# Kernel optimization log

Measured on AMD Instinct MI355X. Metric: run time of the kernel, lower is better.

The kernel has to match this reference:

```python
import jax, jax.numpy as jnp
import numpy as np
import math

B, S, D = 16, 577, 768          # batch, seq (24*24 grid + 1 cls), in_dim=att_dim
H, HD = 12, 64                  # heads, head_dim
GRID = 24                       # height = width; S = GRID*GRID + rpe_skip
RATIO = 1.9
ALPHA, BETA, GAMMA = 1.0 * RATIO, 2.0 * RATIO, 8.0 * RATIO
BETA_INT = int(BETA)            # 3
NUM_BUCKETS = (2 * BETA_INT + 1) ** 2 + 1  # 49 product buckets + 1 extra for skip (cls) = 50


def _piecewise_index(d):
    # iRPE piecewise bucket index (numpy, static). d: integer offsets.
    d = d.astype(np.float64)
    ad = np.abs(d)
    log_part = ALPHA + np.log(np.maximum(ad, 1e-9) / ALPHA) / math.log(GAMMA / ALPHA) * (BETA - ALPHA)
    y_out = np.sign(d) * np.clip(np.round(log_part), None, BETA)
    idx = np.where(ad <= ALPHA, np.round(d), y_out)
    return np.trunc(idx).astype(np.int64)  # torch .to(int) truncates toward zero


def make_rp_bucket():
    # 2D 'product' method bucket ids with skip=1 (cls token -> extra bucket)
    ii, jj = np.meshgrid(np.arange(GRID), np.arange(GRID), indexing='ij')
    pos = np.stack([ii.ravel(), jj.ravel()], axis=-1)          # (L,2)
    diff = pos[:, None, :] - pos[None, :, :]                    # (L,L,2)
    Sb = 2 * BETA_INT + 1
    r = _piecewise_index(diff[..., 0]) + BETA_INT               # [0, 2*beta_int]
    c = _piecewise_index(diff[..., 1]) + BETA_INT
    pid = r * Sb + c                                            # [0, 48]
    L = GRID * GRID
    bucket = np.full((L + 1, L + 1), NUM_BUCKETS - 1, dtype=np.int32)
    bucket[1:, 1:] = pid
    return jnp.asarray(bucket)


def setup_inputs() -> dict:
    key = jax.random.key(0)
    k1, k2, k3 = jax.random.split(key, 3)
    x = jax.random.normal(k1, (B, S, D), dtype=jnp.float32)
    w_qkv = jax.random.normal(k2, (3 * D, D), dtype=jnp.float32) * 0.02   # torch Linear weight (out,in)
    rpe_table = jax.random.normal(k3, (HD, NUM_BUCKETS), dtype=jnp.float32) * 0.02  # shared-head contextual table
    rp_bucket = make_rp_bucket()                                # (S,S) int32
    return {"x": x, "w_qkv": w_qkv, "rpe_table": rpe_table, "rp_bucket": rp_bucket}


def reference(x, w_qkv, rpe_table, rp_bucket):
    qkv = x @ w_qkv.T                                           # (B,S,3D)
    q, k, v = jnp.split(qkv, 3, axis=-1)
    # Faithful to torch source: plain reshape (B,S,D)->(B,H,S,HD) (no transpose-split)
    scale = 1.0 / jnp.sqrt(jnp.asarray(HD, x.dtype))
    q = q.reshape(B, H, S, HD) * scale
    k = k.reshape(B, H, S, HD)
    v = v.reshape(B, H, S, HD)
    qk = jnp.einsum('bhid,bhjd->bhij', q, k)                    # (B,H,S,S)
    # contextual rpe_k: bias[b,h,i,j] = (q[b,h,i] . rpe_table[:, rp_bucket[i,j]])
    ctx = jnp.einsum('bhid,dc->bhic', q, rpe_table)             # (B,H,S,NUM_BUCKETS)
    idx = jnp.broadcast_to(rp_bucket[None, None].astype(jnp.int32), (B, H, S, S))
    bias = jnp.take_along_axis(ctx, idx, axis=-1)               # (B,H,S,S)
    att = jax.nn.softmax(qk + bias, axis=-1)
    out = jnp.einsum('bhij,bhjd->bhid', att, v)                 # (B,H,S,HD)
    y = out.transpose(0, 2, 1, 3).reshape(B, S, D)              # out_proj is Identity (out_dim==att_dim)
    return y
```

## Files before the change

kernel.cpp:

```cpp
#include <hip/hip_runtime.h>

constexpr int BN_  = 16;
constexpr int SN_  = 577;
constexpr int SP_  = 640;
constexpr int DN_  = 768;
constexpr int HN_  = 12;
constexpr int HD_  = 64;
constexpr int NB_  = 50;
constexpr int MR_  = BN_ * SN_;
constexpr int MRP_ = 73 * 128;
constexpr int NQ_  = 3 * DN_;
constexpr int BHS_ = BN_ * HN_ * SN_;
constexpr int SHD_ = SN_ * HD_;

typedef __attribute__((ext_vector_type(8))) short short8;
typedef __attribute__((ext_vector_type(4))) float f32x4;

__device__ __forceinline__ short f2bf(float f) {
  union { float f; unsigned u; } v; v.f = f;
  unsigned r = (v.u + 0x7fffu + ((v.u >> 16) & 1u)) >> 16;
  return (short)r;
}

__device__ __forceinline__ float ex2(float x) {
  float r; asm("v_exp_f32 %0, %1" : "=v"(r) : "v"(x)); return r;
}

__launch_bounds__(256)
__global__ void cvt_k(const float* __restrict__ src, short* __restrict__ dst,
                      int n_src, int n_dst) {
  const int i = (blockIdx.x * 256 + threadIdx.x) * 8;
  if (i >= n_dst) return;
  union { short8 v; short u[8]; } pk;
  if (i < n_src) {
    const float4 a = *(const float4*)(src + i);
    const float4 b = *(const float4*)(src + i + 4);
    pk.u[0] = f2bf(a.x); pk.u[1] = f2bf(a.y); pk.u[2] = f2bf(a.z); pk.u[3] = f2bf(a.w);
    pk.u[4] = f2bf(b.x); pk.u[5] = f2bf(b.y); pk.u[6] = f2bf(b.z); pk.u[7] = f2bf(b.w);
  } else {
#pragma unroll
    for (int j = 0; j < 8; ++j) pk.u[j] = 0;
  }
  *(short8*)(dst + i) = pk.v;
}

__launch_bounds__(256)
__global__ void rpb8_k(const int* __restrict__ rpb, unsigned char* __restrict__ rpbu8) {
  const int tid = blockIdx.x * 256 + threadIdx.x;
  if (tid >= SN_ * 160) return;
  const int i = tid / 160, c4 = tid - i * 160;
  const int j = c4 * 4;
  uchar4 o;
  o.x = (j     < SN_) ? (unsigned char)rpb[i * SN_ + j    ] : 0;
  o.y = (j + 1 < SN_) ? (unsigned char)rpb[i * SN_ + j + 1] : 0;
  o.z = (j + 2 < SN_) ? (unsigned char)rpb[i * SN_ + j + 2] : 0;
  o.w = (j + 3 < SN_) ? (unsigned char)rpb[i * SN_ + j + 3] : 0;
  *(uchar4*)(rpbu8 + (size_t)i * 640 + j) = o;
}

__launch_bounds__(256)
__global__ void qkv_mfma_k(const short* __restrict__ xb, const short* __restrict__ wb,
                           short* __restrict__ Qbf, short* __restrict__ Ksw,
                           short* __restrict__ Vbf) {
  __shared__ short At[128 * 64];
  __shared__ short Bt[128 * 64];
  const int t = threadIdx.x;
  const int w = t >> 6, lane = t & 63, g = lane >> 4, ln = lane & 15;
  const int wm = w >> 1, wn = w & 1;
  const int m0 = blockIdx.y * 128, n0 = blockIdx.x * 128;

  const int sr = t >> 1, su = (t & 1) * 4;
  const short* ga = xb + (size_t)(m0 + sr) * DN_ + su * 8;
  const short* gb = wb + (size_t)(n0 + sr) * DN_ + su * 8;
  short* la = At + sr * 64;
  short* lb = Bt + sr * 64;
  const int swr = sr & 7;

  f32x4 acc[4][4];
#pragma unroll
  for (int mt = 0; mt < 4; ++mt)
#pragma unroll
    for (int nt = 0; nt < 4; ++nt) acc[mt][nt] = (f32x4){0.f, 0.f, 0.f, 0.f};

  short8 ra[4], rb[4];
#pragma unroll
  for (int u = 0; u < 4; ++u) {
    ra[u] = *(const short8*)(ga + u * 8);
    rb[u] = *(const short8*)(gb + u * 8);
  }

  for (int k0 = 0; k0 < DN_; k0 += 64) {
    __syncthreads();
#pragma unroll
    for (int u = 0; u < 4; ++u) {
      *(short8*)(la + (((su + u) ^ swr) * 8)) = ra[u];
      *(short8*)(lb + (((su + u) ^ swr) * 8)) = rb[u];
    }
    __syncthreads();
    if (k0 + 64 < DN_) {
#pragma unroll
      for (int u = 0; u < 4; ++u) {
        ra[u] = *(const short8*)(ga + k0 + 64 + u * 8);
        rb[u] = *(const short8*)(gb + k0 + 64 + u * 8);
      }
    }
#pragma unroll
    for (int kc = 0; kc < 2; ++kc) {
      short8 af[4], bf[4];
#pragma unroll
      for (int mt = 0; mt < 4; ++mt) {
        const int row = wm * 64 + mt * 16 + ln;
        const int u = (kc * 4 + g) ^ (row & 7);
        af[mt] = *(const short8*)&At[row * 64 + u * 8];
      }
#pragma unroll
      for (int nt = 0; nt < 4; ++nt) {
        const int row = wn * 64 + nt * 16 + ln;
        const int u = (kc * 4 + g) ^ (row & 7);
        bf[nt] = *(const short8*)&Bt[row * 64 + u * 8];
      }
#pragma unroll
      for (int mt = 0; mt < 4; ++mt)
#pragma unroll
        for (int nt = 0; nt < 4; ++nt)
          acc[mt][nt] = __builtin_amdgcn_mfma_f32_16x16x32_bf16(af[mt], bf[nt], acc[mt][nt], 0, 0, 0);
    }
  }

  const int nw0  = n0 + wn * 64;
  const int secg = nw0 / DN_;
  const int cbw  = nw0 - secg * DN_;
  const float QSC = 0.18033688011112042f;
#pragma unroll
  for (int mt = 0; mt < 4; ++mt) {
#pragma unroll
    for (int r = 0; r < 4; ++r) {
      const int gm = m0 + wm * 64 + mt * 16 + 4 * g + r;
      if (gm >= MR_) continue;
      const int bb = gm / SN_;
      const int ss = gm - bb * SN_;
      const int pb = ss * DN_ + cbw;
#pragma unroll
      for (int nt = 0; nt < 4; ++nt) {
        const int p   = pb + nt * 16 + ln;
        const int hh  = p / SHD_;
        const int rem = p - hh * SHD_;
        const int ii  = rem >> 6;
        const int dd  = rem & 63;
        const size_t ro = (size_t)(bb * HN_ + hh);
        const float v = acc[mt][nt][r];
        if (secg == 0) {
          Qbf[(ro * SN_ + ii) * 64 + dd] = f2bf(v * QSC);
        } else if (secg == 1) {
          Ksw[(ro * SP_ + ii) * 64 + (dd ^ ((ii & 7) << 3))] = f2bf(v);
        } else {
          Vbf[(ro * SP_ + ii) * 64 + dd] = f2bf(v);
        }
      }
    }
  }
}

__launch_bounds__(256)
__global__ void vtr_k(const short* __restrict__ Vbf, short* __restrict__ Vtsw) {
  __shared__ short T[64][72];
  const int t = threadIdx.x;
  const int jt = blockIdx.x, bh = blockIdx.y;
  const int j0 = jt * 64;
  {
    const int r = t >> 2, c0 = (t & 3) * 16;
    const short* src = Vbf + ((size_t)bh * SP_ + j0 + r) * 64 + c0;
    *(short8*)&T[r][c0]     = *(const short8*)(src);
    *(short8*)&T[r][c0 + 8] = *(const short8*)(src + 8);
  }
  __syncthreads();
  const int d = t >> 2;
  short* dst = Vtsw + ((size_t)bh * 64 + d) * SP_;
  const int sw = (d & 7) << 3;
#pragma unroll
  for (int e = 0; e < 4; ++e) {
    const int jl = (t & 3) * 16 + e * 4;
    const int jg = j0 + jl;
    short4 v;
    v.x = (jg + 0 < SN_) ? T[jl + 0][d] : (short)0;
    v.y = (jg + 1 < SN_) ? T[jl + 1][d] : (short)0;
    v.z = (jg + 2 < SN_) ? T[jl + 2][d] : (short)0;
    v.w = (jg + 3 < SN_) ? T[jl + 3][d] : (short)0;
    *(short4*)&dst[jg ^ sw] = v;
  }
}

__launch_bounds__(256)
__global__ void attn_k(const short* __restrict__ Qbf, const short* __restrict__ Ksw,
                       const short* __restrict__ Vtsw, const float* __restrict__ rpe,
                       const unsigned char* __restrict__ rpbu8, float* __restrict__ y) {
  __shared__ short Kt[64 * 64];
  __shared__ short Vt[64 * 64];
  __shared__ float ctxs[4][16][53];
  __shared__ char urp[8192];
  short (*Rp)[64] = (short (*)[64])urp;
  unsigned char* rpbt = (unsigned char*)urp;

  const int t = threadIdx.x;
  const int w = t >> 6, lane = t & 63, g = lane >> 4, ln = lane & 15;
  const int qt = blockIdx.x, bh = blockIdx.y;
  const int b = bh / HN_, h = bh - b * HN_;
  const int i0 = qt * 64;
  const size_t rb = (size_t)bh * SN_;
  const short* Kbh = Ksw + (size_t)bh * SP_ * 64;
  const short* Vbh = Vtsw + (size_t)bh * 64 * SP_;

  const int sr_ = t >> 2, scu_ = (t & 3) * 16;
  const int irow_s = (i0 + sr_ <= SN_ - 1) ? (i0 + sr_) : (SN_ - 1);

  short8 kr0, kr1, vr0, vr1; int4 rp_;
  {
    const short* ks = Kbh + (size_t)sr_ * 64 + scu_;
    kr0 = *(const short8*)(ks); kr1 = *(const short8*)(ks + 8);
    const short* vs = Vbh + (size_t)sr_ * SP_ + scu_;
    vr0 = *(const short8*)(vs); vr1 = *(const short8*)(vs + 8);
    rp_ = *(const int4*)(rpbu8 + (size_t)irow_s * 640 + scu_);
  }

  for (int e = t; e < 64 * 64; e += 256) {
    const int c = e >> 6, d = e & 63;
    Rp[c][d] = (c < NB_) ? f2bf(rpe[d * NB_ + c]) : (short)0;
  }

  short8 qf[2];
  {
    int row = i0 + 16 * w + ln; if (row > SN_ - 1) row = SN_ - 1;
    const short* qp = Qbf + (rb + row) * 64;
    qf[0] = *(const short8*)(qp + 8 * g);
    qf[1] = *(const short8*)(qp + 32 + 8 * g);
  }

  __syncthreads();

  {
    f32x4 accC[4];
#pragma unroll
    for (int ct = 0; ct < 4; ++ct) accC[ct] = (f32x4){0.f, 0.f, 0.f, 0.f};
#pragma unroll
    for (int kc = 0; kc < 2; ++kc) {
#pragma unroll
      for (int ct = 0; ct < 4; ++ct) {
        const short8 rf = *(const short8*)&Rp[ct * 16 + ln][kc * 32 + 8 * g];
        accC[ct] = __builtin_amdgcn_mfma_f32_16x16x32_bf16(qf[kc], rf, accC[ct], 0, 0, 0);
      }
    }
#pragma unroll
    for (int ct = 0; ct < 4; ++ct) {
      const int c = ct * 16 + ln;
      if (c < 53) {
#pragma unroll
        for (int r = 0; r < 4; ++r) ctxs[w][4 * g + r][c] = accC[ct][r];
      }
    }
  }

  float m = -3e38f, l = 0.f;
  f32x4 accO[4];
#pragma unroll
  for (int dt = 0; dt < 4; ++dt) accO[dt] = (f32x4){0.f, 0.f, 0.f, 0.f};

  const int swv = (ln & 7) << 3;
  const float* cbase = &ctxs[w][ln][0];
  const int rpoff = (16 * w + ln) * 80;

  for (int jt = 0; jt < 10; ++jt) {
    const int j0 = jt * 64;
    __syncthreads();
    *(short8*)&Kt[sr_ * 64 + scu_]     = kr0;
    *(short8*)&Kt[sr_ * 64 + scu_ + 8] = kr1;
    *(short8*)&Vt[sr_ * 64 + scu_]     = vr0;
    *(short8*)&Vt[sr_ * 64 + scu_ + 8] = vr1;
    *(int4*)&rpbt[sr_ * 80 + scu_]     = rp_;
    __syncthreads();

    if (jt < 9) {
      const int jn = j0 + 64;
      const short* ks = Kbh + (size_t)(jn + sr_) * 64 + scu_;
      kr0 = *(const short8*)(ks); kr1 = *(const short8*)(ks + 8);
      const short* vs = Vbh + (size_t)sr_ * SP_ + jn + scu_;
      vr0 = *(const short8*)(vs); vr1 = *(const short8*)(vs + 8);
      rp_ = *(const int4*)(rpbu8 + (size_t)irow_s * 640 + jn + scu_);
    }

    f32x4 accS[4];
#pragma unroll
    for (int nt = 0; nt < 4; ++nt) accS[nt] = (f32x4){0.f, 0.f, 0.f, 0.f};
#pragma unroll
    for (int kc = 0; kc < 2; ++kc) {
      const int cb = (kc * 32 + 8 * g) ^ swv;
#pragma unroll
      for (int nt = 0; nt < 4; ++nt) {
        const short8 kf = *(const short8*)&Kt[(nt * 16 + ln) * 64 + cb];
        accS[nt] = __builtin_amdgcn_mfma_f32_16x16x32_bf16(kf, qf[kc], accS[nt], 0, 0, 0);
      }
    }

    float pv[4][4];
#pragma unroll
    for (int nt = 0; nt < 4; ++nt) {
      const uchar4 bk = *(const uchar4*)&rpbt[rpoff + nt * 16 + 4 * g];
      pv[nt][0] = accS[nt][0] + cbase[bk.x];
      pv[nt][1] = accS[nt][1] + cbase[bk.y];
      pv[nt][2] = accS[nt][2] + cbase[bk.z];
      pv[nt][3] = accS[nt][3] + cbase[bk.w];
    }
    if (jt == 9) {
#pragma unroll
      for (int nt = 0; nt < 4; ++nt) {
        const int jb = j0 + nt * 16 + 4 * g;
#pragma unroll
        for (int r = 0; r < 4; ++r)
          if (jb + r >= SN_) pv[nt][r] = -3e38f;
      }
    }

    float mx = fmaxf(fmaxf(pv[0][0], pv[0][1]), fmaxf(pv[0][2], pv[0][3]));
#pragma unroll
    for (int nt = 1; nt < 4; ++nt)
      mx = fmaxf(mx, fmaxf(fmaxf(pv[nt][0], pv[nt][1]), fmaxf(pv[nt][2], pv[nt][3])));
    mx = fmaxf(mx, __shfl_xor(mx, 16));
    mx = fmaxf(mx, __shfl_xor(mx, 32));

    if (__any(mx > m + 8.f)) {
      const float mnew = fmaxf(m, mx);
      const float sc = ex2(m - mnew);
      float scr[4];
#pragma unroll
      for (int r = 0; r < 4; ++r) scr[r] = __shfl(sc, 4 * g + r);
#pragma unroll
      for (int dt = 0; dt < 4; ++dt)
#pragma unroll
        for (int r = 0; r < 4; ++r) accO[dt][r] *= scr[r];
      l *= sc;
      m = mnew;
    }

    float sum = 0.f;
#pragma unroll
    for (int nt = 0; nt < 4; ++nt)
#pragma unroll
      for (int r = 0; r < 4; ++r) {
        const float p = ex2(pv[nt][r] - m);
        pv[nt][r] = p;
        sum += p;
      }
    sum += __shfl_xor(sum, 16);
    sum += __shfl_xor(sum, 32);
    l += sum;

    short8 pf[2];
#pragma unroll
    for (int kc = 0; kc < 2; ++kc) {
      union { short8 v; short u[8]; } pk;
#pragma unroll
      for (int r = 0; r < 4; ++r) {
        pk.u[r]     = f2bf(pv[2 * kc][r]);
        pk.u[4 + r] = f2bf(pv[2 * kc + 1][r]);
      }
      pf[kc] = pk.v;
    }

#pragma unroll
    for (int kc = 0; kc < 2; ++kc) {
#pragma unroll
      for (int dt = 0; dt < 4; ++dt) {
        const short* vrow = &Vt[(dt * 16 + ln) * 64];
        union { short8 v; short4 hh[2]; } u;
        u.hh[0] = *(const short4*)&vrow[(kc * 32 + 4 * g) ^ swv];
        u.hh[1] = *(const short4*)&vrow[(kc * 32 + 16 + 4 * g) ^ swv];
        accO[dt] = __builtin_amdgcn_mfma_f32_16x16x32_bf16(pf[kc], u.v, accO[dt], 0, 0, 0);
      }
    }
  }

  float linv[4];
#pragma unroll
  for (int r = 0; r < 4; ++r) linv[r] = 1.f / __shfl(l, 4 * g + r);
#pragma unroll
  for (int r = 0; r < 4; ++r) {
    const int i = i0 + 16 * w + 4 * g + r;
    if (i >= SN_) continue;
    float* yp = y + ((size_t)b * SN_ + i) * DN_ + h * HD_ + ln;
#pragma unroll
    for (int dt = 0; dt < 4; ++dt) yp[dt * 16] = accO[dt][r] * linv[r];
  }
}

extern "C" void kernel_launch(void* const* d_in, const int* in_sizes, int n_in,
                              void* d_out, int out_size, void* d_ws, size_t ws_size,
                              hipStream_t stream) {
  const float* x   = (const float*)d_in[0];
  const float* w   = (const float*)d_in[1];
  const float* rpe = (const float*)d_in[2];
  const int*   rpb = (const int*)d_in[3];
  float* y = (float*)d_out;

  short* xb   = (short*)d_ws;
  short* wb   = xb + (size_t)MRP_ * DN_;
  short* Qbf  = wb + (size_t)NQ_ * DN_;
  short* Ksw  = Qbf + (size_t)BHS_ * HD_;
  short* Vbf  = Ksw + (size_t)BN_ * HN_ * SP_ * 64;
  short* Vtsw = Vbf + (size_t)BN_ * HN_ * SP_ * 64;
  unsigned char* rpbu8 = (unsigned char*)(Vtsw + (size_t)BN_ * HN_ * 64 * SP_);

  cvt_k<<<dim3(MRP_ * DN_ / 2048), 256, 0, stream>>>(x, xb, MR_ * DN_, MRP_ * DN_);
  cvt_k<<<dim3(NQ_ * DN_ / 2048), 256, 0, stream>>>(w, wb, NQ_ * DN_, NQ_ * DN_);
  rpb8_k<<<dim3((SN_ * 160 + 255) / 256), 256, 0, stream>>>(rpb, rpbu8);
  qkv_mfma_k<<<dim3(18, 73), 256, 0, stream>>>(xb, wb, Qbf, Ksw, Vbf);
  vtr_k<<<dim3(10, BN_ * HN_), 256, 0, stream>>>(Vbf, Vtsw);
  attn_k<<<dim3(10, BN_ * HN_), 256, 0, stream>>>(Qbf, Ksw, Vtsw, rpe, rpbu8, y);
}
```

Before: 160.4 us.

## Widen attention blocks to 128 query rows with 8 waves sharing K/V tiles

Each attention block now uses 512 threads and handles 128 query rows instead of 64, so every K/V tile staged in shared memory is reused by twice as many waves and the total K/V global traffic is halved. The grid drops from 10 to 5 query tiles per head, and the row stride of the bucket-index tile shrinks to fit the larger per-block layout. The bf16 packing of probabilities now uses the packed hardware convert instruction, and the MFMA sections are wrapped in wave-priority raises. The risks are fewer blocks (960 vs 1920) with more padding waste in the last tile, and higher LDS use per block, which may reduce occupancy.

After: 173.1 us. 7.9% more time.

```diff
diff --git a/kernel.cpp b/kernel.cpp
--- a/kernel.cpp
+++ b/kernel.cpp
@@ -24,6 +24,11 @@
 
 __device__ __forceinline__ float ex2(float x) {
   float r; asm("v_exp_f32 %0, %1" : "=v"(r) : "v"(x)); return r;
+}
+
+__device__ __forceinline__ unsigned cvtpk(float a, float b) {
+  unsigned r; asm("v_cvt_pk_bf16_f32 %0, %1, %2" : "=v"(r) : "v"(a), "v"(b));
+  return r;
 }
 
 __launch_bounds__(256)
@@ -190,14 +195,14 @@
   }
 }
 
-__launch_bounds__(256)
+__launch_bounds__(512, 6)
 __global__ void attn_k(const short* __restrict__ Qbf, const short* __restrict__ Ksw,
                        const short* __restrict__ Vtsw, const float* __restrict__ rpe,
                        const unsigned char* __restrict__ rpbu8, float* __restrict__ y) {
   __shared__ short Kt[64 * 64];
   __shared__ short Vt[64 * 64];
-  __shared__ float ctxs[4][16][53];
-  __shared__ char urp[8192];
+  __shared__ float ctxs[8][16][53];
+  __shared__ char urp[9216];
   short (*Rp)[64] = (short (*)[64])urp;
   unsigned char* rpbt = (unsigned char*)urp;
 
@@ -205,24 +210,23 @@
   const int w = t >> 6, lane = t & 63, g = lane >> 4, ln = lane & 15;
   const int qt = blockIdx.x, bh = blockIdx.y;
   const int b = bh / HN_, h = bh - b * HN_;
-  const int i0 = qt * 64;
+  const int i0 = qt * 128;
   const size_t rb = (size_t)bh * SN_;
   const short* Kbh = Ksw + (size_t)bh * SP_ * 64;
   const short* Vbh = Vtsw + (size_t)bh * 64 * SP_;
 
-  const int sr_ = t >> 2, scu_ = (t & 3) * 16;
-  const int irow_s = (i0 + sr_ <= SN_ - 1) ? (i0 + sr_) : (SN_ - 1);
-
-  short8 kr0, kr1, vr0, vr1; int4 rp_;
+  const int kvr_ = t >> 3, kvc_ = (t & 7) * 8;
+  const int rpr_ = t >> 2, rpc_ = (t & 3) * 16;
+  const int irow_s = (i0 + rpr_ <= SN_ - 1) ? (i0 + rpr_) : (SN_ - 1);
+
+  short8 kr_, vr_; int4 rp_;
   {
-    const short* ks = Kbh + (size_t)sr_ * 64 + scu_;
-    kr0 = *(const short8*)(ks); kr1 = *(const short8*)(ks + 8);
-    const short* vs = Vbh + (size_t)sr_ * SP_ + scu_;
-    vr0 = *(const short8*)(vs); vr1 = *(const short8*)(vs + 8);
-    rp_ = *(const int4*)(rpbu8 + (size_t)irow_s * 640 + scu_);
-  }
-
-  for (int e = t; e < 64 * 64; e += 256) {
+    kr_ = *(const short8*)(Kbh + (size_t)kvr_ * 64 + kvc_);
+    vr_ = *(const short8*)(Vbh + (size_t)kvr_ * SP_ + kvc_);
+    rp_ = *(const int4*)(rpbu8 + (size_t)irow_s * 640 + rpc_);
+  }
+
+  for (int e = t; e < 64 * 64; e += 512) {
     const int c = e >> 6, d = e & 63;
     Rp[c][d] = (c < NB_) ? f2bf(rpe[d * NB_ + c]) : (short)0;
   }
@@ -266,30 +270,31 @@
 
   const int swv = (ln & 7) << 3;
   const float* cbase = &ctxs[w][ln][0];
-  const int rpoff = (16 * w + ln) * 80;
+  const int rpoff = (16 * w + ln) * 72;
 
   for (int jt = 0; jt < 10; ++jt) {
     const int j0 = jt * 64;
     __syncthreads();
-    *(short8*)&Kt[sr_ * 64 + scu_]     = kr0;
-    *(short8*)&Kt[sr_ * 64 + scu_ + 8] = kr1;
-    *(short8*)&Vt[sr_ * 64 + scu_]     = vr0;
-    *(short8*)&Vt[sr_ * 64 + scu_ + 8] = vr1;
-    *(int4*)&rpbt[sr_ * 80 + scu_]     = rp_;
+    *(short8*)&Kt[kvr_ * 64 + kvc_] = kr_;
+    *(short8*)&Vt[kvr_ * 64 + kvc_] = vr_;
+    {
+      const int o = rpr_ * 72 + rpc_;
+      *(int2*)&rpbt[o]     = make_int2(rp_.x, rp_.y);
+      *(int2*)&rpbt[o + 8] = make_int2(rp_.z, rp_.w);
+    }
     __syncthreads();
 
     if (jt < 9) {
       const int jn = j0 + 64;
-      const short* ks = Kbh + (size_t)(jn + sr_) * 64 + scu_;
-      kr0 = *(const short8*)(ks); kr1 = *(const short8*)(ks + 8);
-      const short* vs = Vbh + (size_t)sr_ * SP_ + jn + scu_;
-      vr0 = *(const short8*)(vs); vr1 = *(const short8*)(vs + 8);
-      rp_ = *(const int4*)(rpbu8 + (size_t)irow_s * 640 + jn + scu_);
+      kr_ = *(const short8*)(Kbh + (size_t)(jn + kvr_) * 64 + kvc_);
+      vr_ = *(const short8*)(Vbh + (size_t)kvr_ * SP_ + jn + kvc_);
+      rp_ = *(const int4*)(rpbu8 + (size_t)irow_s * 640 + jn + rpc_);
     }
 
     f32x4 accS[4];
 #pragma unroll
     for (int nt = 0; nt < 4; ++nt) accS[nt] = (f32x4){0.f, 0.f, 0.f, 0.f};
+    __builtin_amdgcn_s_setprio(1);
 #pragma unroll
     for (int kc = 0; kc < 2; ++kc) {
       const int cb = (kc * 32 + 8 * g) ^ swv;
@@ -299,6 +304,7 @@
         accS[nt] = __builtin_amdgcn_mfma_f32_16x16x32_bf16(kf, qf[kc], accS[nt], 0, 0, 0);
       }
     }
+    __builtin_amdgcn_s_setprio(0);
 
     float pv[4][4];
 #pragma unroll
@@ -356,15 +362,15 @@
     short8 pf[2];
 #pragma unroll
     for (int kc = 0; kc < 2; ++kc) {
-      union { short8 v; short u[8]; } pk;
-#pragma unroll
-      for (int r = 0; r < 4; ++r) {
-        pk.u[r]     = f2bf(pv[2 * kc][r]);
-        pk.u[4 + r] = f2bf(pv[2 * kc + 1][r]);
-      }
+      union { short8 v; unsigned wd[4]; } pk;
+      pk.wd[0] = cvtpk(pv[2 * kc][0],     pv[2 * kc][1]);
+      pk.wd[1] = cvtpk(pv[2 * kc][2],     pv[2 * kc][3]);
+      pk.wd[2] = cvtpk(pv[2 * kc + 1][0], pv[2 * kc + 1][1]);
+      pk.wd[3] = cvtpk(pv[2 * kc + 1][2], pv[2 * kc + 1][3]);
       pf[kc] = pk.v;
     }
 
+    __builtin_amdgcn_s_setprio(1);
 #pragma unroll
     for (int kc = 0; kc < 2; ++kc) {
 #pragma unroll
@@ -376,6 +382,7 @@
         accO[dt] = __builtin_amdgcn_mfma_f32_16x16x32_bf16(pf[kc], u.v, accO[dt], 0, 0, 0);
       }
     }
+    __builtin_amdgcn_s_setprio(0);
   }
 
   float linv[4];
@@ -413,5 +420,5 @@
   rpb8_k<<<dim3((SN_ * 160 + 255) / 256), 256, 0, stream>>>(rpb, rpbu8);
   qkv_mfma_k<<<dim3(18, 73), 256, 0, stream>>>(xb, wb, Qbf, Ksw, Vbf);
   vtr_k<<<dim3(10, BN_ * HN_), 256, 0, stream>>>(Vbf, Vtsw);
-  attn_k<<<dim3(10, BN_ * HN_), 256, 0, stream>>>(Qbf, Ksw, Vtsw, rpe, rpbu8, y);
-}
+  attn_k<<<dim3(5, BN_ * HN_), 512, 0, stream>>>(Qbf, Ksw, Vtsw, rpe, rpbu8, y);
+}
```
